# Kernel tuning notes

Hardware: AMD Instinct MI355X
Metric: run time of the kernel (lower is better)

## Reference

```python
import jax, jax.numpy as jnp
import numpy as np

B, T, C = 2, 2048, 1024
N_HEAD = 16
HEAD_DIM = C // N_HEAD


def setup_inputs() -> dict:
    key = jax.random.key(0)
    k1, k2, k3 = jax.random.split(key, 3)
    x = jax.random.normal(k1, (B, T, C), dtype=jnp.float32)
    # broadcastable causal mask: 1 where attendable, 0 where masked
    mask = jnp.tril(jnp.ones((T, T), dtype=jnp.int32))[None, None, :, :]
    W_qkv = jax.random.normal(k2, (C, 3 * C), dtype=jnp.float32) * (1.0 / np.sqrt(C))
    b_qkv = jnp.zeros((3 * C,), dtype=jnp.float32)
    W_out = jax.random.normal(k3, (C, C), dtype=jnp.float32) * (1.0 / np.sqrt(C))
    b_out = jnp.zeros((C,), dtype=jnp.float32)
    return {"x": x, "mask": mask, "W_qkv": W_qkv, "b_qkv": b_qkv, "W_out": W_out, "b_out": b_out}


def reference(x, mask, W_qkv, b_qkv, W_out, b_out):
    Bx, Tx, Cx = x.shape
    # fused QKV projection
    qkv = x @ W_qkv + b_qkv  # [B, T, 3C]
    qkv = qkv.reshape(Bx, Tx, 3, N_HEAD, HEAD_DIM).transpose(2, 0, 3, 1, 4)  # [3, B, H, T, D]
    q, k, v = qkv[0], qkv[1], qkv[2]
    scale = 1.0 / jnp.sqrt(jnp.asarray(HEAD_DIM, dtype=x.dtype))
    att = jnp.einsum('bhqd,bhkd->bhqk', q, k) * scale  # [B, H, T, T]
    att = jnp.where(mask == 0, -jnp.inf, att)
    att = jax.nn.softmax(att, axis=-1)
    # dropout is deterministic=True in the original -> identity
    y = jnp.einsum('bhqk,bhkd->bhqd', att, v)  # [B, H, T, D]
    y = y.transpose(0, 2, 1, 3).reshape(Bx, Tx, Cx)
    return y @ W_out + b_out
```

## Files before the change

kernel.cpp:

```cpp
#include <hip/hip_runtime.h>
#include <hip/hip_bf16.h>
#include <math.h>

#define B_  2
#define T_  2048
#define C_  1024
#define NH  16
#define HD  64

typedef __attribute__((ext_vector_type(8))) short short8;
typedef __attribute__((ext_vector_type(4))) float f32x4;

__device__ __forceinline__ void gload_lds16(const void* g, void* l) {
    __builtin_amdgcn_global_load_lds(
        (const __attribute__((address_space(1))) void*)g,
        (__attribute__((address_space(3))) void*)l, 16, 0, 0);
}

__device__ __forceinline__ unsigned short f2bf(float f) {
    __hip_bfloat16 b = __float2bfloat16(f);
    return *reinterpret_cast<unsigned short*>(&b);
}

__global__ __launch_bounds__(256) void cast_bf16_kernel(
    const float* __restrict__ in, __hip_bfloat16* __restrict__ out, int n4)
{
    const int i = blockIdx.x * 256 + threadIdx.x;
    if (i >= n4) return;
    const float4 v = reinterpret_cast<const float4*>(in)[i];
    ushort4 o;
    o.x = f2bf(v.x); o.y = f2bf(v.y); o.z = f2bf(v.z); o.w = f2bf(v.w);
    reinterpret_cast<ushort4*>(out)[i] = o;
}

__global__ __launch_bounds__(256) void transpose_cast_kernel(
    const float* __restrict__ W, __hip_bfloat16* __restrict__ Wt, int R, int Ccols)
{
    __shared__ float tile[32][33];
    const int c0 = blockIdx.x * 32, r0 = blockIdx.y * 32;
    const int tx = threadIdx.x & 31, ty = threadIdx.x >> 5;
    #pragma unroll
    for (int i = 0; i < 32; i += 8)
        tile[ty + i][tx] = W[(size_t)(r0 + ty + i) * Ccols + c0 + tx];
    __syncthreads();
    #pragma unroll
    for (int i = 0; i < 32; i += 8)
        Wt[(size_t)(c0 + ty + i) * R + r0 + tx] = __float2bfloat16(tile[tx][ty + i]);
}

#define QBM 256
#define QBN 256
#define QBK 32

__global__ __launch_bounds__(512) void gemm_bf16_8ph(
    const __hip_bfloat16* __restrict__ A,
    const __hip_bfloat16* __restrict__ Bt,
    const float* __restrict__ bias,
    __hip_bfloat16* __restrict__ Cb,
    __hip_bfloat16* __restrict__ vt,
    int M, int N, int K, int gx)
{
    __shared__ __align__(16) __hip_bfloat16 As[4][QBM * QBK];
    __shared__ __align__(16) __hip_bfloat16 Bs[4][QBN * QBK];

    const int nwg = (int)gridDim.x;
    const int orig = (int)blockIdx.x;
    const int qq = nwg >> 3, rr = nwg & 7;
    const int xcd = orig & 7, off = orig >> 3;
    const int wgid = (xcd < rr ? xcd * (qq + 1)
                               : rr * (qq + 1) + (xcd - rr) * qq) + off;
    const int bx = wgid % gx;
    const int by = wgid / gx;

    const int tid = threadIdx.x;
    const int w = tid >> 6, lane = tid & 63;
    const int wm = w >> 2, wn = w & 3;
    const int lr = lane & 15, kb = lane >> 4;

    const size_t rowA0 = (size_t)by * QBM;
    const size_t colB0 = (size_t)bx * QBN;

    const int rS   = tid >> 2;
    const int blkl = tid & 3;
    const int bsw  = blkl ^ ((rS >> 1) & 3);
    const __hip_bfloat16* gA0 = A  + (rowA0 + rS) * K + bsw * 8;
    const __hip_bfloat16* gA1 = gA0 + (size_t)128 * K;
    const __hip_bfloat16* gB0 = Bt + (colB0 + rS) * K + bsw * 8;
    const __hip_bfloat16* gB1 = gB0 + (size_t)128 * K;

    const int NT = K / QBK;

    #define STAGE_A(t) { char* d = (char*)As[(t) & 3] + tid * 16;            \
        gload_lds16(gA0 + (t) * QBK, d);                                     \
        gload_lds16(gA1 + (t) * QBK, d + 8192); }
    #define STAGE_B(t) { char* d = (char*)Bs[(t) & 3] + tid * 16;            \
        gload_lds16(gB0 + (t) * QBK, d);                                     \
        gload_lds16(gB1 + (t) * QBK, d + 8192); }

    const int rowAl = wm * 128 + lr;
    const int rowBl = wn * 64 + lr;
    const int ofsA = rowAl * 64 + (kb ^ ((rowAl >> 1) & 3)) * 16;
    const int ofsB = rowBl * 64 + (kb ^ ((rowBl >> 1) & 3)) * 16;

    f32x4 acc[8][4];
    #pragma unroll
    for (int i = 0; i < 8; ++i)
        #pragma unroll
        for (int j = 0; j < 4; ++j)
            acc[i][j] = (f32x4){0.f, 0.f, 0.f, 0.f};

    STAGE_A(0); STAGE_B(0);
    STAGE_A(1); STAGE_B(1);
    STAGE_A(2); STAGE_B(2);

    for (int t = 0; t < NT; ++t) {
        if (t + 2 < NT)      asm volatile("s_waitcnt vmcnt(8)" ::: "memory");
        else if (t + 1 < NT) asm volatile("s_waitcnt vmcnt(4)" ::: "memory");
        else                 asm volatile("s_waitcnt vmcnt(0)" ::: "memory");
        __builtin_amdgcn_s_barrier();
        __builtin_amdgcn_sched_barrier(0);

        const char* Ab = (const char*)As[t & 3];
        const char* Bb = (const char*)Bs[t & 3];

        short8 bf[4], af[4];
        #pragma unroll
        for (int j = 0; j < 4; ++j)
            bf[j] = *reinterpret_cast<const short8*>(Bb + ofsB + 1024 * j);
        #pragma unroll
        for (int i = 0; i < 4; ++i)
            af[i] = *reinterpret_cast<const short8*>(Ab + ofsA + 1024 * i);
        if (t + 3 < NT) STAGE_A(t + 3);
        __builtin_amdgcn_s_setprio(1);
        #pragma unroll
        for (int i = 0; i < 4; ++i)
            #pragma unroll
            for (int j = 0; j < 4; ++j)
                acc[i][j] = __builtin_amdgcn_mfma_f32_16x16x32_bf16(
                    af[i], bf[j], acc[i][j], 0, 0, 0);
        __builtin_amdgcn_s_setprio(0);

        __builtin_amdgcn_s_barrier();
        __builtin_amdgcn_sched_barrier(0);
        #pragma unroll
        for (int i = 0; i < 4; ++i)
            af[i] = *reinterpret_cast<const short8*>(Ab + ofsA + 1024 * (i + 4));
        if (t + 3 < NT) STAGE_B(t + 3);
        __builtin_amdgcn_s_setprio(1);
        #pragma unroll
        for (int i = 0; i < 4; ++i)
            #pragma unroll
            for (int j = 0; j < 4; ++j)
                acc[i + 4][j] = __builtin_amdgcn_mfma_f32_16x16x32_bf16(
                    af[i], bf[j], acc[i + 4][j], 0, 0, 0);
        __builtin_amdgcn_s_setprio(0);
    }

    const int orow4 = (lane >> 4) * 4;
    #pragma unroll
    for (int i = 0; i < 8; ++i) {
        #pragma unroll
        for (int j = 0; j < 4; ++j) {
            const size_t col = colB0 + wn * 64 + j * 16 + lr;
            const float bb = bias[col];
            float v[4];
            #pragma unroll
            for (int r = 0; r < 4; ++r) v[r] = acc[i][j][r] + bb;
            const size_t row0 = rowA0 + wm * 128 + i * 16 + orow4;
            #pragma unroll
            for (int r = 0; r < 4; ++r)
                Cb[(row0 + r) * N + col] = __float2bfloat16(v[r]);
            if (vt && (int)col >= 2 * C_) {
                const int vc = (int)col - 2 * C_;
                const int hh = vc >> 6, dd = vc & 63;
                const int bb_ = (int)(row0 >> 11);
                const int t0  = (int)(row0 & 2047);
                ushort4 o;
                o.x = f2bf(v[0]); o.y = f2bf(v[1]); o.z = f2bf(v[2]); o.w = f2bf(v[3]);
                *reinterpret_cast<ushort4*>(
                    vt + (((size_t)(bb_ * NH + hh) * 64 + dd) * T_ + t0)) = o;
            }
        }
    }
    #undef STAGE_A
    #undef STAGE_B
}

#define GBM 128
#define GBN 128
#define GBK 64

__global__ __launch_bounds__(256) void gemm_bf16_mfma(
    const __hip_bfloat16* __restrict__ A,
    const __hip_bfloat16* __restrict__ Bt,
    const float* __restrict__ bias,
    float* __restrict__ Cf,
    int M, int N, int K, int gx)
{
    __shared__ __align__(16) __hip_bfloat16 As[GBM * GBK];
    __shared__ __align__(16) __hip_bfloat16 Bs[GBN * GBK];

    const int nwg = (int)gridDim.x;
    const int orig = (int)blockIdx.x;
    const int qq = nwg >> 3, rr = nwg & 7;
    const int xcd = orig & 7, off = orig >> 3;
    const int wgid = (xcd < rr ? xcd * (qq + 1)
                               : rr * (qq + 1) + (xcd - rr) * qq) + off;
    const int bx = wgid % gx;
    const int by = wgid / gx;

    const int tid = threadIdx.x;
    const int lane = tid & 63;
    const int wid = tid >> 6;
    const int wr = wid >> 1, wc = wid & 1;
    const int lr = lane & 15;
    const int lk = (lane >> 4) * 8;

    const size_t rowA0 = (size_t)by * GBM;
    const size_t colB0 = (size_t)bx * GBN;

    f32x4 acc[4][4];
    #pragma unroll
    for (int i = 0; i < 4; ++i)
        #pragma unroll
        for (int j = 0; j < 4; ++j)
            acc[i][j] = (f32x4){0.f, 0.f, 0.f, 0.f};

    for (int k0 = 0; k0 < K; k0 += GBK) {
        #pragma unroll
        for (int it = 0; it < 4; ++it) {
            const int idx = tid + it * 256;
            const int r  = idx >> 3;
            const int kc = (idx & 7) * 8;
            gload_lds16(A  + (rowA0 + r) * K + k0 + kc, &As[idx * 8]);
            gload_lds16(Bt + (colB0 + r) * K + k0 + kc, &Bs[idx * 8]);
        }
        __syncthreads();

        #pragma unroll
        for (int kk = 0; kk < GBK; kk += 32) {
            short8 af[4], bf[4];
            #pragma unroll
            for (int i = 0; i < 4; ++i)
                af[i] = *reinterpret_cast<const short8*>(
                    &As[(wr * 64 + i * 16 + lr) * GBK + kk + lk]);
            #pragma unroll
            for (int j = 0; j < 4; ++j)
                bf[j] = *reinterpret_cast<const short8*>(
                    &Bs[(wc * 64 + j * 16 + lr) * GBK + kk + lk]);
            #pragma unroll
            for (int i = 0; i < 4; ++i)
                #pragma unroll
                for (int j = 0; j < 4; ++j)
                    acc[i][j] = __builtin_amdgcn_mfma_f32_16x16x32_bf16(
                        af[i], bf[j], acc[i][j], 0, 0, 0);
        }
        __syncthreads();
    }

    const int orow = (lane >> 4) * 4;
    #pragma unroll
    for (int i = 0; i < 4; ++i) {
        #pragma unroll
        for (int j = 0; j < 4; ++j) {
            const size_t col = colB0 + wc * 64 + j * 16 + lr;
            const float bb = bias[col];
            #pragma unroll
            for (int r = 0; r < 4; ++r) {
                const size_t row = rowA0 + wr * 64 + i * 16 + orow + r;
                Cf[row * N + col] = acc[i][j][r] + bb;
            }
        }
    }
}

__global__ __launch_bounds__(256) void attn_mfma_kernel(
    const __hip_bfloat16* __restrict__ qkvb,
    const __hip_bfloat16* __restrict__ vtg,
    __hip_bfloat16* __restrict__ yb)
{
    const int bh = blockIdx.x;
    const int b = bh >> 4, h = bh & 15;
    const int qt = (int)gridDim.y - 1 - (int)blockIdx.y;
    const int tid = threadIdx.x;
    const int w = tid >> 6, lane = tid & 63;
    const int lr = lane & 15, lg = lane >> 4;

    __shared__ __align__(16) __hip_bfloat16 Ks[2][64 * 64];
    __shared__ __align__(16) __hip_bfloat16 Vts[2][64 * 64];
    __shared__ __align__(16) __hip_bfloat16 Pl[4][16 * 64];

    const int qrow = qt * 64 + w * 16;
    const size_t s3C = 3 * C_;

    const float qscale = 0.125f * 1.44269504f;
    const __hip_bfloat16* qp =
        qkvb + ((size_t)(b * T_) + qrow + lr) * s3C + h * 64 + lg * 8;
    short8 qf0 = *reinterpret_cast<const short8*>(qp);
    short8 qf1 = *reinterpret_cast<const short8*>(qp + 32);
    #pragma unroll
    for (int j = 0; j < 8; ++j) {
        const float f0 = __uint_as_float(((unsigned)(unsigned short)qf0[j]) << 16);
        const float f1 = __uint_as_float(((unsigned)(unsigned short)qf1[j]) << 16);
        qf0[j] = (short)f2bf(f0 * qscale);
        qf1[j] = (short)f2bf(f1 * qscale);
    }

    short8 vone;
    #pragma unroll
    for (int j = 0; j < 8; ++j) vone[j] = (lr == 0) ? (short)0x3F80 : (short)0;

    f32x4 o_acc[5];
    #pragma unroll
    for (int db = 0; db < 5; ++db) o_acc[db] = (f32x4){0.f, 0.f, 0.f, 0.f};

    char* PlB = (char*)Pl[w];

    auto STAGE = [&](int t, int bi) {
        #pragma unroll
        for (int rr = 0; rr < 2; ++rr) {
            const int slot = (rr * 4 + w) * 64 + lane;
            const int row = slot >> 3;
            const int gblk = (slot & 7) ^ (row & 7);
            gload_lds16(qkvb + ((size_t)(b * T_) + t * 64 + row) * s3C
                             + C_ + h * 64 + gblk * 8,
                        (char*)Ks[bi] + slot * 16);
            gload_lds16(vtg + ((size_t)bh * 64 + row) * T_ + t * 64 + gblk * 8,
                        (char*)Vts[bi] + slot * 16);
        }
    };

    STAGE(0, 0);
    __syncthreads();
    int buf = 0;

    for (int t = 0; t <= qt; ++t) {
        if (t < qt) STAGE(t + 1, buf ^ 1);

        const char* KsB  = (const char*)Ks[buf];
        const char* VtsB = (const char*)Vts[buf];

        f32x4 sacc[4];
        #pragma unroll
        for (int kb = 0; kb < 4; ++kb) sacc[kb] = (f32x4){0.f, 0.f, 0.f, 0.f};
        __builtin_amdgcn_s_setprio(1);
        #pragma unroll
        for (int kb = 0; kb < 4; ++kb) {
            const int key = kb * 16 + lr;
            const short8 kf0 = *reinterpret_cast<const short8*>(
                KsB + key * 128 + ((lg) ^ (key & 7)) * 16);
            const short8 kf1 = *reinterpret_cast<const short8*>(
                KsB + key * 128 + ((4 + lg) ^ (key & 7)) * 16);
            sacc[kb] = __builtin_amdgcn_mfma_f32_16x16x32_bf16(qf0, kf0, sacc[kb], 0, 0, 0);
            sacc[kb] = __builtin_amdgcn_mfma_f32_16x16x32_bf16(qf1, kf1, sacc[kb], 0, 0, 0);
        }
        __builtin_amdgcn_s_setprio(0);

        const bool diag = (t == qt);
        #pragma unroll
        for (int r = 0; r < 4; ++r) {
            const int qlocal = lg * 4 + r;
            #pragma unroll
            for (int kb = 0; kb < 4; ++kb) {
                float s = sacc[kb][r];
                if (diag) {
                    const int keyg = t * 64 + kb * 16 + lr;
                    s = (keyg <= qrow + qlocal) ? s : -INFINITY;
                }
                const float p = exp2f(s);
                const int key = kb * 16 + lr;
                const int byte = qlocal * 128
                               + (((key >> 3) ^ (qlocal & 7)) * 16) + (key & 7) * 2;
                *reinterpret_cast<__hip_bfloat16*>(PlB + byte) = __float2bfloat16(p);
            }
        }

        const short8 pf0 = *reinterpret_cast<const short8*>(
            PlB + lr * 128 + ((lg) ^ (lr & 7)) * 16);
        const short8 pf1 = *reinterpret_cast<const short8*>(
            PlB + lr * 128 + ((4 + lg) ^ (lr & 7)) * 16);
        __builtin_amdgcn_s_setprio(1);
        #pragma unroll
        for (int db = 0; db < 4; ++db) {
            const int dd = db * 16 + lr;
            const short8 vf0 = *reinterpret_cast<const short8*>(
                VtsB + dd * 128 + ((lg) ^ (dd & 7)) * 16);
            const short8 vf1 = *reinterpret_cast<const short8*>(
                VtsB + dd * 128 + ((4 + lg) ^ (dd & 7)) * 16);
            o_acc[db] = __builtin_amdgcn_mfma_f32_16x16x32_bf16(pf0, vf0, o_acc[db], 0, 0, 0);
            o_acc[db] = __builtin_amdgcn_mfma_f32_16x16x32_bf16(pf1, vf1, o_acc[db], 0, 0, 0);
        }
        o_acc[4] = __builtin_amdgcn_mfma_f32_16x16x32_bf16(pf0, vone, o_acc[4], 0, 0, 0);
        o_acc[4] = __builtin_amdgcn_mfma_f32_16x16x32_bf16(pf1, vone, o_acc[4], 0, 0, 0);
        __builtin_amdgcn_s_setprio(0);

        __syncthreads();
        buf ^= 1;
    }

    #pragma unroll
    for (int r = 0; r < 4; ++r) {
        const float lsum = __shfl(o_acc[4][r], (lane & 48));
        const float inv = 1.f / lsum;
        const int qg = qrow + lg * 4 + r;
        __hip_bfloat16* yp = yb + ((size_t)(b * T_) + qg) * C_ + h * 64;
        #pragma unroll
        for (int db = 0; db < 4; ++db)
            yp[db * 16 + lr] = __float2bfloat16(o_acc[db][r] * inv);
    }
}

extern "C" void kernel_launch(void* const* d_in, const int* in_sizes, int n_in,
                              void* d_out, int out_size, void* d_ws, size_t ws_size,
                              hipStream_t stream)
{
    const float* x     = (const float*)d_in[0];
    const float* W_qkv = (const float*)d_in[2];
    const float* b_qkv = (const float*)d_in[3];
    const float* W_out = (const float*)d_in[4];
    const float* b_out = (const float*)d_in[5];
    float* out = (float*)d_out;

    __hip_bfloat16* qkvb = (__hip_bfloat16*)d_ws;
    __hip_bfloat16* vtg  = qkvb + (size_t)B_ * T_ * 3 * C_;
    __hip_bfloat16* xb   = vtg  + (size_t)B_ * NH * 64 * T_;
    __hip_bfloat16* wqt  = xb   + (size_t)B_ * T_ * C_;
    __hip_bfloat16* wot  = wqt  + (size_t)3 * C_ * C_;
    __hip_bfloat16* yb   = wot  + (size_t)C_ * C_;

    const int M = B_ * T_;

    cast_bf16_kernel<<<(M * C_ / 4 + 255) / 256, 256, 0, stream>>>(x, xb, M * C_ / 4);
    {
        dim3 g(3 * C_ / 32, C_ / 32);
        transpose_cast_kernel<<<g, 256, 0, stream>>>(W_qkv, wqt, C_, 3 * C_);
    }
    {
        dim3 g(C_ / 32, C_ / 32);
        transpose_cast_kernel<<<g, 256, 0, stream>>>(W_out, wot, C_, C_);
    }

    {
        const int gx = 3 * C_ / QBN, gy = M / QBM;
        gemm_bf16_8ph<<<dim3(gx * gy), 512, 0, stream>>>(
            xb, wqt, b_qkv, qkvb, vtg, M, 3 * C_, C_, gx);
    }
    {
        dim3 grid(B_ * NH, T_ / 64);
        attn_mfma_kernel<<<grid, 256, 0, stream>>>(qkvb, vtg, yb);
    }
    {
        const int gx = C_ / GBN, gy = M / GBM;
        gemm_bf16_mfma<<<dim3(gx * gy), 256, 0, stream>>>(
            yb, wot, b_out, out, M, C_, C_, gx);
    }
}
```

Measured before the change: 203.9 us.

## Switch attention kernel to 32x32x16 MFMA with two waves per block

Rewrites the attention kernel to use 32x32x16 bf16 MFMA tiles, so each of two waves handles 32 query rows instead of four waves handling 16. The row sum is now accumulated in registers from the fp32 probabilities and reduced with xor-shuffles, replacing the extra MFMA against a ones vector. A truncating-round bf16 conversion replaces the library conversion for P and the output. This reduces LDS fragment reloads and MFMA issue count per tile, but halves the threads per block and raises register pressure, which can reduce latency hiding.

Result: slower. 223.1 us (+9.4%).

```diff
diff --git a/kernel.cpp b/kernel.cpp
--- a/kernel.cpp
+++ b/kernel.cpp
@@ -8,8 +8,9 @@
 #define NH  16
 #define HD  64
 
-typedef __attribute__((ext_vector_type(8))) short short8;
-typedef __attribute__((ext_vector_type(4))) float f32x4;
+typedef __attribute__((ext_vector_type(8)))  short short8;
+typedef __attribute__((ext_vector_type(4)))  float f32x4;
+typedef __attribute__((ext_vector_type(16))) float f32x16;
 
 __device__ __forceinline__ void gload_lds16(const void* g, void* l) {
     __builtin_amdgcn_global_load_lds(
@@ -20,6 +21,9 @@
 __device__ __forceinline__ unsigned short f2bf(float f) {
     __hip_bfloat16 b = __float2bfloat16(f);
     return *reinterpret_cast<unsigned short*>(&b);
+}
+__device__ __forceinline__ unsigned short f2bf_fast(float f) {
+    return (unsigned short)((__float_as_uint(f) + 0x8000u) >> 16);
 }
 
 __global__ __launch_bounds__(256) void cast_bf16_kernel(
@@ -274,7 +278,7 @@
     }
 }
 
-__global__ __launch_bounds__(256) void attn_mfma_kernel(
+__global__ __launch_bounds__(128) void attn_mfma_kernel(
     const __hip_bfloat16* __restrict__ qkvb,
     const __hip_bfloat16* __restrict__ vtg,
     __hip_bfloat16* __restrict__ yb)
@@ -283,43 +287,42 @@
     const int b = bh >> 4, h = bh & 15;
     const int qt = (int)gridDim.y - 1 - (int)blockIdx.y;
     const int tid = threadIdx.x;
-    const int w = tid >> 6, lane = tid & 63;
-    const int lr = lane & 15, lg = lane >> 4;
+    const int w = tid >> 6;
+    const int lane = tid & 63;
+    const int l31 = lane & 31, g = lane >> 5;
 
     __shared__ __align__(16) __hip_bfloat16 Ks[2][64 * 64];
     __shared__ __align__(16) __hip_bfloat16 Vts[2][64 * 64];
-    __shared__ __align__(16) __hip_bfloat16 Pl[4][16 * 64];
-
-    const int qrow = qt * 64 + w * 16;
+    __shared__ __align__(16) __hip_bfloat16 Pl[2][32 * 64];
+
+    const int qrow = qt * 64 + w * 32;
     const size_t s3C = 3 * C_;
 
     const float qscale = 0.125f * 1.44269504f;
     const __hip_bfloat16* qp =
-        qkvb + ((size_t)(b * T_) + qrow + lr) * s3C + h * 64 + lg * 8;
-    short8 qf0 = *reinterpret_cast<const short8*>(qp);
-    short8 qf1 = *reinterpret_cast<const short8*>(qp + 32);
-    #pragma unroll
-    for (int j = 0; j < 8; ++j) {
-        const float f0 = __uint_as_float(((unsigned)(unsigned short)qf0[j]) << 16);
-        const float f1 = __uint_as_float(((unsigned)(unsigned short)qf1[j]) << 16);
-        qf0[j] = (short)f2bf(f0 * qscale);
-        qf1[j] = (short)f2bf(f1 * qscale);
-    }
-
-    short8 vone;
-    #pragma unroll
-    for (int j = 0; j < 8; ++j) vone[j] = (lr == 0) ? (short)0x3F80 : (short)0;
-
-    f32x4 o_acc[5];
-    #pragma unroll
-    for (int db = 0; db < 5; ++db) o_acc[db] = (f32x4){0.f, 0.f, 0.f, 0.f};
+        qkvb + ((size_t)(b * T_) + qrow + l31) * s3C + h * 64 + g * 8;
+    short8 qa[4];
+    #pragma unroll
+    for (int s = 0; s < 4; ++s) {
+        qa[s] = *reinterpret_cast<const short8*>(qp + s * 16);
+        #pragma unroll
+        for (int j = 0; j < 8; ++j) {
+            const float f = __uint_as_float(((unsigned)(unsigned short)qa[s][j]) << 16);
+            qa[s][j] = (short)f2bf(f * qscale);
+        }
+    }
+
+    f32x16 o0 = {}, o1 = {};
+    float lp[16];
+    #pragma unroll
+    for (int i = 0; i < 16; ++i) lp[i] = 0.f;
 
     char* PlB = (char*)Pl[w];
 
     auto STAGE = [&](int t, int bi) {
         #pragma unroll
-        for (int rr = 0; rr < 2; ++rr) {
-            const int slot = (rr * 4 + w) * 64 + lane;
+        for (int rr = 0; rr < 4; ++rr) {
+            const int slot = rr * 128 + tid;
             const int row = slot >> 3;
             const int gblk = (slot & 7) ^ (row & 7);
             gload_lds16(qkvb + ((size_t)(b * T_) + t * 64 + row) * s3C
@@ -340,58 +343,51 @@
         const char* KsB  = (const char*)Ks[buf];
         const char* VtsB = (const char*)Vts[buf];
 
-        f32x4 sacc[4];
-        #pragma unroll
-        for (int kb = 0; kb < 4; ++kb) sacc[kb] = (f32x4){0.f, 0.f, 0.f, 0.f};
+        f32x16 s0 = {}, s1 = {};
         __builtin_amdgcn_s_setprio(1);
         #pragma unroll
-        for (int kb = 0; kb < 4; ++kb) {
-            const int key = kb * 16 + lr;
+        for (int s = 0; s < 4; ++s) {
+            const int blk = (s * 2 + g) ^ (l31 & 7);
             const short8 kf0 = *reinterpret_cast<const short8*>(
-                KsB + key * 128 + ((lg) ^ (key & 7)) * 16);
+                KsB + l31 * 128 + blk * 16);
             const short8 kf1 = *reinterpret_cast<const short8*>(
-                KsB + key * 128 + ((4 + lg) ^ (key & 7)) * 16);
-            sacc[kb] = __builtin_amdgcn_mfma_f32_16x16x32_bf16(qf0, kf0, sacc[kb], 0, 0, 0);
-            sacc[kb] = __builtin_amdgcn_mfma_f32_16x16x32_bf16(qf1, kf1, sacc[kb], 0, 0, 0);
+                KsB + (32 + l31) * 128 + blk * 16);
+            s0 = __builtin_amdgcn_mfma_f32_32x32x16_bf16(qa[s], kf0, s0, 0, 0, 0);
+            s1 = __builtin_amdgcn_mfma_f32_32x32x16_bf16(qa[s], kf1, s1, 0, 0, 0);
         }
         __builtin_amdgcn_s_setprio(0);
 
         const bool diag = (t == qt);
         #pragma unroll
-        for (int r = 0; r < 4; ++r) {
-            const int qlocal = lg * 4 + r;
-            #pragma unroll
-            for (int kb = 0; kb < 4; ++kb) {
-                float s = sacc[kb][r];
-                if (diag) {
-                    const int keyg = t * 64 + kb * 16 + lr;
-                    s = (keyg <= qrow + qlocal) ? s : -INFINITY;
-                }
-                const float p = exp2f(s);
-                const int key = kb * 16 + lr;
-                const int byte = qlocal * 128
-                               + (((key >> 3) ^ (qlocal & 7)) * 16) + (key & 7) * 2;
-                *reinterpret_cast<__hip_bfloat16*>(PlB + byte) = __float2bfloat16(p);
+        for (int reg = 0; reg < 16; ++reg) {
+            const int row = (reg & 3) + 8 * (reg >> 2) + 4 * g;
+            float v0 = s0[reg], v1 = s1[reg];
+            if (diag) {
+                const int qg = w * 32 + row;
+                v0 = (l31 <= qg)      ? v0 : -INFINITY;
+                v1 = (32 + l31 <= qg) ? v1 : -INFINITY;
             }
-        }
-
-        const short8 pf0 = *reinterpret_cast<const short8*>(
-            PlB + lr * 128 + ((lg) ^ (lr & 7)) * 16);
-        const short8 pf1 = *reinterpret_cast<const short8*>(
-            PlB + lr * 128 + ((4 + lg) ^ (lr & 7)) * 16);
+            const float p0 = exp2f(v0);
+            const float p1 = exp2f(v1);
+            lp[reg] += p0 + p1;
+            const int a0 = row * 128 + (((l31 >> 3) ^ (row & 7)) * 16) + (l31 & 7) * 2;
+            *reinterpret_cast<unsigned short*>(PlB + a0)        = f2bf_fast(p0);
+            *reinterpret_cast<unsigned short*>(PlB + (a0 ^ 64)) = f2bf_fast(p1);
+        }
+
         __builtin_amdgcn_s_setprio(1);
         #pragma unroll
-        for (int db = 0; db < 4; ++db) {
-            const int dd = db * 16 + lr;
+        for (int s = 0; s < 4; ++s) {
+            const int blk = (s * 2 + g) ^ (l31 & 7);
+            const short8 pa = *reinterpret_cast<const short8*>(
+                PlB + l31 * 128 + blk * 16);
             const short8 vf0 = *reinterpret_cast<const short8*>(
-                VtsB + dd * 128 + ((lg) ^ (dd & 7)) * 16);
+                VtsB + l31 * 128 + blk * 16);
             const short8 vf1 = *reinterpret_cast<const short8*>(
-                VtsB + dd * 128 + ((4 + lg) ^ (dd & 7)) * 16);
-            o_acc[db] = __builtin_amdgcn_mfma_f32_16x16x32_bf16(pf0, vf0, o_acc[db], 0, 0, 0);
-            o_acc[db] = __builtin_amdgcn_mfma_f32_16x16x32_bf16(pf1, vf1, o_acc[db], 0, 0, 0);
-        }
-        o_acc[4] = __builtin_amdgcn_mfma_f32_16x16x32_bf16(pf0, vone, o_acc[4], 0, 0, 0);
-        o_acc[4] = __builtin_amdgcn_mfma_f32_16x16x32_bf16(pf1, vone, o_acc[4], 0, 0, 0);
+                VtsB + (32 + l31) * 128 + blk * 16);
+            o0 = __builtin_amdgcn_mfma_f32_32x32x16_bf16(pa, vf0, o0, 0, 0, 0);
+            o1 = __builtin_amdgcn_mfma_f32_32x32x16_bf16(pa, vf1, o1, 0, 0, 0);
+        }
         __builtin_amdgcn_s_setprio(0);
 
         __syncthreads();
@@ -399,14 +395,23 @@
     }
 
     #pragma unroll
-    for (int r = 0; r < 4; ++r) {
-        const float lsum = __shfl(o_acc[4][r], (lane & 48));
-        const float inv = 1.f / lsum;
-        const int qg = qrow + lg * 4 + r;
+    for (int reg = 0; reg < 16; ++reg) {
+        float v = lp[reg];
+        v += __shfl_xor(v, 1);
+        v += __shfl_xor(v, 2);
+        v += __shfl_xor(v, 4);
+        v += __shfl_xor(v, 8);
+        v += __shfl_xor(v, 16);
+        lp[reg] = 1.f / v;
+    }
+
+    #pragma unroll
+    for (int reg = 0; reg < 16; ++reg) {
+        const int row = (reg & 3) + 8 * (reg >> 2) + 4 * g;
+        const int qg = qrow + row;
         __hip_bfloat16* yp = yb + ((size_t)(b * T_) + qg) * C_ + h * 64;
-        #pragma unroll
-        for (int db = 0; db < 4; ++db)
-            yp[db * 16 + lr] = __float2bfloat16(o_acc[db][r] * inv);
+        *reinterpret_cast<unsigned short*>(yp + l31)      = f2bf_fast(o0[reg] * lp[reg]);
+        *reinterpret_cast<unsigned short*>(yp + 32 + l31) = f2bf_fast(o1[reg] * lp[reg]);
     }
 }
 
@@ -447,7 +452,7 @@
     }
     {
         dim3 grid(B_ * NH, T_ / 64);
-        attn_mfma_kernel<<<grid, 256, 0, stream>>>(qkvb, vtg, yb);
+        attn_mfma_kernel<<<grid, 128, 0, stream>>>(qkvb, vtg, yb);
     }
     {
         const int gx = C_ / GBN, gy = M / GBM;
```

## Load K and V fragments directly from global memory into registers in attention

Applied to the files above, without the earlier changes.

The attention kernel no longer stages K and V tiles through double-buffered LDS with global_load_lds. Each wave now reads its own K and V^T MFMA fragments straight from global memory into registers, prefetching the next K tile during the softmax. This removes the per-iteration block barrier and the LDS traffic. In exchange, the four waves each fetch the same K/V data redundantly from global memory or L2, and the V loads are issued at the start of each iteration, which can expose load latency.

New measurement: 293.2 us. 1.44x slower.

```diff
diff --git a/kernel.cpp b/kernel.cpp
--- a/kernel.cpp
+++ b/kernel.cpp
@@ -8,8 +8,8 @@
 #define NH  16
 #define HD  64
 
-typedef __attribute__((ext_vector_type(8))) short short8;
-typedef __attribute__((ext_vector_type(4))) float f32x4;
+typedef __attribute__((ext_vector_type(8)))  short short8;
+typedef __attribute__((ext_vector_type(4)))  float f32x4;
 
 __device__ __forceinline__ void gload_lds16(const void* g, void* l) {
     __builtin_amdgcn_global_load_lds(
@@ -286,8 +286,6 @@
     const int w = tid >> 6, lane = tid & 63;
     const int lr = lane & 15, lg = lane >> 4;
 
-    __shared__ __align__(16) __hip_bfloat16 Ks[2][64 * 64];
-    __shared__ __align__(16) __hip_bfloat16 Vts[2][64 * 64];
     __shared__ __align__(16) __hip_bfloat16 Pl[4][16 * 64];
 
     const int qrow = qt * 64 + w * 16;
@@ -316,29 +314,33 @@
 
     char* PlB = (char*)Pl[w];
 
-    auto STAGE = [&](int t, int bi) {
-        #pragma unroll
-        for (int rr = 0; rr < 2; ++rr) {
-            const int slot = (rr * 4 + w) * 64 + lane;
-            const int row = slot >> 3;
-            const int gblk = (slot & 7) ^ (row & 7);
-            gload_lds16(qkvb + ((size_t)(b * T_) + t * 64 + row) * s3C
-                             + C_ + h * 64 + gblk * 8,
-                        (char*)Ks[bi] + slot * 16);
-            gload_lds16(vtg + ((size_t)bh * 64 + row) * T_ + t * 64 + gblk * 8,
-                        (char*)Vts[bi] + slot * 16);
-        }
-    };
-
-    STAGE(0, 0);
-    __syncthreads();
-    int buf = 0;
+    const __hip_bfloat16* kp[4];
+    #pragma unroll
+    for (int kb = 0; kb < 4; ++kb)
+        kp[kb] = qkvb + ((size_t)(b * T_) + kb * 16 + lr) * s3C
+               + C_ + h * 64 + lg * 8;
+    const __hip_bfloat16* vp[4];
+    #pragma unroll
+    for (int db = 0; db < 4; ++db)
+        vp[db] = vtg + ((size_t)bh * 64 + db * 16 + lr) * T_ + lg * 8;
+
+    const size_t kstep = (size_t)64 * s3C;
+
+    short8 kf[8];
+    #pragma unroll
+    for (int kb = 0; kb < 4; ++kb) {
+        kf[kb]     = *reinterpret_cast<const short8*>(kp[kb]);
+        kf[kb + 4] = *reinterpret_cast<const short8*>(kp[kb] + 32);
+    }
 
     for (int t = 0; t <= qt; ++t) {
-        if (t < qt) STAGE(t + 1, buf ^ 1);
-
-        const char* KsB  = (const char*)Ks[buf];
-        const char* VtsB = (const char*)Vts[buf];
+        short8 vf[8];
+        #pragma unroll
+        for (int db = 0; db < 4; ++db) {
+            vf[db]     = *reinterpret_cast<const short8*>(vp[db]);
+            vf[db + 4] = *reinterpret_cast<const short8*>(vp[db] + 32);
+            vp[db] += 64;
+        }
 
         f32x4 sacc[4];
         #pragma unroll
@@ -346,15 +348,19 @@
         __builtin_amdgcn_s_setprio(1);
         #pragma unroll
         for (int kb = 0; kb < 4; ++kb) {
-            const int key = kb * 16 + lr;
-            const short8 kf0 = *reinterpret_cast<const short8*>(
-                KsB + key * 128 + ((lg) ^ (key & 7)) * 16);
-            const short8 kf1 = *reinterpret_cast<const short8*>(
-                KsB + key * 128 + ((4 + lg) ^ (key & 7)) * 16);
-            sacc[kb] = __builtin_amdgcn_mfma_f32_16x16x32_bf16(qf0, kf0, sacc[kb], 0, 0, 0);
-            sacc[kb] = __builtin_amdgcn_mfma_f32_16x16x32_bf16(qf1, kf1, sacc[kb], 0, 0, 0);
+            sacc[kb] = __builtin_amdgcn_mfma_f32_16x16x32_bf16(qf0, kf[kb],     sacc[kb], 0, 0, 0);
+            sacc[kb] = __builtin_amdgcn_mfma_f32_16x16x32_bf16(qf1, kf[kb + 4], sacc[kb], 0, 0, 0);
         }
         __builtin_amdgcn_s_setprio(0);
+
+        if (t < qt) {
+            #pragma unroll
+            for (int kb = 0; kb < 4; ++kb) {
+                kp[kb] += kstep;
+                kf[kb]     = *reinterpret_cast<const short8*>(kp[kb]);
+                kf[kb + 4] = *reinterpret_cast<const short8*>(kp[kb] + 32);
+            }
+        }
 
         const bool diag = (t == qt);
         #pragma unroll
@@ -382,20 +388,12 @@
         __builtin_amdgcn_s_setprio(1);
         #pragma unroll
         for (int db = 0; db < 4; ++db) {
-            const int dd = db * 16 + lr;
-            const short8 vf0 = *reinterpret_cast<const short8*>(
-                VtsB + dd * 128 + ((lg) ^ (dd & 7)) * 16);
-            const short8 vf1 = *reinterpret_cast<const short8*>(
-                VtsB + dd * 128 + ((4 + lg) ^ (dd & 7)) * 16);
-            o_acc[db] = __builtin_amdgcn_mfma_f32_16x16x32_bf16(pf0, vf0, o_acc[db], 0, 0, 0);
-            o_acc[db] = __builtin_amdgcn_mfma_f32_16x16x32_bf16(pf1, vf1, o_acc[db], 0, 0, 0);
+            o_acc[db] = __builtin_amdgcn_mfma_f32_16x16x32_bf16(pf0, vf[db],     o_acc[db], 0, 0, 0);
+            o_acc[db] = __builtin_amdgcn_mfma_f32_16x16x32_bf16(pf1, vf[db + 4], o_acc[db], 0, 0, 0);
         }
         o_acc[4] = __builtin_amdgcn_mfma_f32_16x16x32_bf16(pf0, vone, o_acc[4], 0, 0, 0);
         o_acc[4] = __builtin_amdgcn_mfma_f32_16x16x32_bf16(pf1, vone, o_acc[4], 0, 0, 0);
         __builtin_amdgcn_s_setprio(0);
-
-        __syncthreads();
-        buf ^= 1;
     }
 
     #pragma unroll
```
